# Optimization experiments

Measured on AMD Instinct MI355X. Metric: run time of the kernel, lower is better.

Reference implementation:

```python
import jax, jax.numpy as jnp
import numpy as np

B, T, D = 8, 2048, 1024  # batch, seq (== block_size), n_embd == head_size


def setup_inputs() -> dict:
    key = jax.random.key(0)
    k0, k1, k2, k3 = jax.random.split(key, 4)
    s = 1.0 / np.sqrt(D)
    return {
        "x": jax.random.normal(k0, (B, T, D), dtype=jnp.float32),
        "Wk": jax.random.normal(k1, (D, D), dtype=jnp.float32) * s,
        "Wq": jax.random.normal(k2, (D, D), dtype=jnp.float32) * s,
        "Wv": jax.random.normal(k3, (D, D), dtype=jnp.float32) * s,
    }


def reference(x, Wk, Wq, Wv):
    Bb, Tt, C = x.shape
    k = jnp.einsum("btc,ch->bth", x, Wk)
    q = jnp.einsum("btc,ch->bth", x, Wq)
    v = jnp.einsum("btc,ch->bth", x, Wv)
    # scaled dot-product scores with causal (tril) mask; scale = C**-0.5 (n_embd)
    wei = jnp.einsum("bqh,bkh->bqk", q, k) * (1.0 / jnp.sqrt(jnp.float32(C)))
    causal = jnp.tril(jnp.ones((Tt, Tt), dtype=bool))
    wei = jnp.where(causal[None, :, :], wei, jnp.float32(-jnp.inf))
    wei = jax.nn.softmax(wei, axis=-1)
    # dropout is identity in eval mode
    out = jnp.einsum("bqk,bkh->bqh", wei, v)
    return out
```

## Files before the change

kernel.cpp:

```cpp
#include <hip/hip_runtime.h>
#include <hip/hip_bf16.h>

#define BB 8
#define TT 2048
#define DD 1024

typedef __attribute__((ext_vector_type(8))) short short8;
typedef __attribute__((ext_vector_type(4))) float f32x4;
typedef __attribute__((ext_vector_type(4))) unsigned short u16x4;

__device__ inline void gload_lds16(const void* g, void* l) {
    __builtin_amdgcn_global_load_lds((const __attribute__((address_space(1))) void*)g,
                                     (__attribute__((address_space(3))) void*)l, 16, 0, 0);
}

#define VMW4 asm volatile("s_waitcnt vmcnt(4)" ::: "memory")
#define VMW0 asm volatile("s_waitcnt vmcnt(0)" ::: "memory")
#define BARX() __builtin_amdgcn_s_barrier()

#define MM_PAIR(NF0)                                                          \
    do {                                                                      \
        __builtin_amdgcn_s_setprio(1);                                        \
        _Pragma("unroll")                                                     \
        for (int mf = 0; mf < 8; mf++) {                                      \
            acc[mf][NF0] = __builtin_amdgcn_mfma_f32_16x16x32_bf16(           \
                aF[mf], bF[NF0], acc[mf][NF0], 0, 0, 0);                      \
            acc[mf][NF0 + 1] = __builtin_amdgcn_mfma_f32_16x16x32_bf16(       \
                aF[mf], bF[NF0 + 1], acc[mf][NF0 + 1], 0, 0, 0);              \
        }                                                                     \
        __builtin_amdgcn_s_setprio(0);                                        \
    } while (0)

template<int MODE, typename CT>
__device__ __forceinline__ void gemm_core256(
    const __hip_bfloat16* __restrict__ A,
    const __hip_bfloat16* __restrict__ Bt,
    void* __restrict__ Cbase,
    int lda, int ldb, int ldc,
    int m0, int n0, int kmax,
    float scale, float* __restrict__ rs)
{
    __shared__ __align__(16) char lsA[65536];
    __shared__ __align__(16) char lsB[65536];

    const int t   = threadIdx.x;
    const int w   = t >> 6;
    const int l   = t & 63;
    const int q   = l >> 4;
    const int i16 = l & 15;
    const int wy  = w >> 2;
    const int wx  = w & 3;

    const int r0  = w * 32 + (l >> 2);
    const int r1  = r0 + 16;
    const int cg0 = (l & 3) ^ ((r0 >> 1) & 3);
    const int cg1 = (l & 3) ^ ((r1 >> 1) & 3);
    const __hip_bfloat16* gA0 = A  + (size_t)(m0 + r0) * lda + cg0 * 8;
    const __hip_bfloat16* gA1 = A  + (size_t)(m0 + r1) * lda + cg1 * 8;
    const __hip_bfloat16* gB0 = Bt + (size_t)(n0 + r0) * ldb + cg0 * 8;
    const __hip_bfloat16* gB1 = Bt + (size_t)(n0 + r1) * ldb + cg1 * 8;

    const int swz  = (q ^ ((i16 >> 1) & 3)) << 4;
    const int offA = (wy * 128 + i16) * 64 + swz;
    const int offB = (wx * 64  + i16) * 64 + swz;

    f32x4 acc[8][4];
#pragma unroll
    for (int mf = 0; mf < 8; mf++)
#pragma unroll
        for (int nf = 0; nf < 4; nf++) acc[mf][nf] = f32x4{0.f, 0.f, 0.f, 0.f};

    short8 aF[8], bF[4];
    const int NT = kmax >> 6;

    {
        char* dA = lsA + (w << 11);
        char* dB = lsB + (w << 11);
        gload_lds16(gA0, dA);            gload_lds16(gA1, dA + 1024);
        gload_lds16(gB0, dB);            gload_lds16(gB1, dB + 1024);
        gload_lds16(gA0 + 32, dA + 16384); gload_lds16(gA1 + 32, dA + 16384 + 1024);
        gload_lds16(gB0 + 32, dB + 16384); gload_lds16(gB1 + 32, dB + 16384 + 1024);
    }
    VMW4; BARX();

    int buf = 0;
    for (int tt = 0; tt < NT; ++tt, buf ^= 1) {
        const bool nx = (tt + 1) < NT;
        const int  kn = (tt + 1) << 6;
        char* sA = lsA + (buf ? 32768 : 0);
        char* sB = lsB + (buf ? 32768 : 0);
        char* dA = lsA + (buf ? 0 : 32768) + (w << 11);
        char* dB = lsB + (buf ? 0 : 32768) + (w << 11);

#pragma unroll
        for (int mf = 0; mf < 8; mf++)
            aF[mf] = *(const short8*)(sA + offA + mf * 1024);
#pragma unroll
        for (int nf = 0; nf < 4; nf++)
            bF[nf] = *(const short8*)(sB + offB + nf * 1024);
        if (nx) { gload_lds16(gA0 + kn, dA); gload_lds16(gA1 + kn, dA + 1024); }
        BARX();
        MM_PAIR(0);
        BARX();
        if (nx) { gload_lds16(gB0 + kn, dB); gload_lds16(gB1 + kn, dB + 1024); }
        BARX();
        MM_PAIR(2);
        if (nx) { VMW4; } else { VMW0; }
        BARX();
#pragma unroll
        for (int mf = 0; mf < 8; mf++)
            aF[mf] = *(const short8*)(sA + 16384 + offA + mf * 1024);
#pragma unroll
        for (int nf = 0; nf < 4; nf++)
            bF[nf] = *(const short8*)(sB + 16384 + offB + nf * 1024);
        if (nx) { gload_lds16(gA0 + kn + 32, dA + 16384);
                  gload_lds16(gA1 + kn + 32, dA + 16384 + 1024); }
        BARX();
        MM_PAIR(0);
        BARX();
        if (nx) { gload_lds16(gB0 + kn + 32, dB + 16384);
                  gload_lds16(gB1 + kn + 32, dB + 16384 + 1024); }
        BARX();
        MM_PAIR(2);
        if (nx) { VMW4; }
        BARX();
    }

    if constexpr (MODE == 0) {
        CT* C = (CT*)Cbase;
#pragma unroll
        for (int mf = 0; mf < 8; mf++) {
            int rbase = m0 + wy * 128 + mf * 16 + q * 4;
#pragma unroll
            for (int nf = 0; nf < 4; nf++) {
                int col = n0 + wx * 64 + nf * 16 + i16;
#pragma unroll
                for (int r = 0; r < 4; r++) {
                    float v = acc[mf][nf][r] * scale;
                    if constexpr (sizeof(CT) == 2)
                        C[(size_t)(rbase + r) * ldc + col] = (CT)__float2bfloat16(v);
                    else
                        *((float*)&C[(size_t)(rbase + r) * ldc + col]) = v;
                }
            }
        }
    } else if constexpr (MODE == 1) {
        __hip_bfloat16* C = (__hip_bfloat16*)Cbase;
#pragma unroll
        for (int mf = 0; mf < 8; mf++) {
            int rbase = m0 + wy * 128 + mf * 16 + q * 4;
#pragma unroll
            for (int r = 0; r < 4; r++) {
                int row = rbase + r;
                float part = 0.f, pv[4];
#pragma unroll
                for (int nf = 0; nf < 4; nf++) {
                    int col = n0 + wx * 64 + nf * 16 + i16;
                    float e = (col <= row) ? __expf(acc[mf][nf][r] * scale) : 0.f;
                    pv[nf] = e;
                    part += e;
                }
                part += __shfl_xor(part, 1, 64);
                part += __shfl_xor(part, 2, 64);
                part += __shfl_xor(part, 4, 64);
                part += __shfl_xor(part, 8, 64);
                if (i16 == 0) atomicAdd(&rs[row], part);
#pragma unroll
                for (int nf = 0; nf < 4; nf++) {
                    int col = n0 + wx * 64 + nf * 16 + i16;
                    C[(size_t)row * ldc + col] = __float2bfloat16(pv[nf]);
                }
            }
        }
    } else {
        float* C = (float*)Cbase;
#pragma unroll
        for (int mf = 0; mf < 8; mf++) {
            int rbase = m0 + wy * 128 + mf * 16 + q * 4;
#pragma unroll
            for (int r = 0; r < 4; r++) {
                int row = rbase + r;
                float inv = 1.f / rs[row];
#pragma unroll
                for (int nf = 0; nf < 4; nf++) {
                    int col = n0 + wx * 64 + nf * 16 + i16;
                    C[(size_t)row * ldc + col] = acc[mf][nf][r] * inv;
                }
            }
        }
    }
}

__global__ __launch_bounds__(512, 2) void proj3_8ph(
    const __hip_bfloat16* __restrict__ xb,
    const __hip_bfloat16* __restrict__ wt,
    __hip_bfloat16* __restrict__ kq,
    __hip_bfloat16* __restrict__ vT2)
{
    const int z = blockIdx.y;
    const int x = blockIdx.x;
    const int swz = (x & 7) * 32 + (x >> 3);
    const __hip_bfloat16 *A, *Bt;
    void* C;
    int ldc, m0, n0;
    if (z < 2) {
        A = xb; Bt = wt + z * 1048576; C = kq + (size_t)z * 16777216;
        ldc = 1024; m0 = (swz >> 2) * 256; n0 = (swz & 3) * 256;
    } else {
        A = wt + 2 * 1048576; Bt = xb; C = vT2;
        ldc = 16384; m0 = (swz & 3) * 256; n0 = (swz >> 2) * 256;
    }
    gemm_core256<0, __hip_bfloat16>(A, Bt, C, 1024, 1024, ldc, m0, n0, 1024, 1.0f, nullptr);
}

__global__ __launch_bounds__(512, 2) void sgemm256(
    const __hip_bfloat16* __restrict__ qq,
    const __hip_bfloat16* __restrict__ kk,
    __hip_bfloat16* __restrict__ Pp,
    float* __restrict__ rsum)
{
    const int z = blockIdx.z;
    const int y = blockIdx.y;
    const int ne = ((y + z) & 1) ? blockIdx.x : 7 - blockIdx.x;
    if (ne > y) return;
    gemm_core256<1, __hip_bfloat16>(
        qq + (size_t)z * 2097152, kk + (size_t)z * 2097152,
        Pp + (size_t)z * 4194304,
        1024, 1024, 2048, y * 256, ne * 256, 1024, 0.03125f,
        rsum + (size_t)z * TT);
}

__global__ __launch_bounds__(512, 2) void pvgemm256(
    const __hip_bfloat16* __restrict__ Pp,
    const __hip_bfloat16* __restrict__ vT2,
    float* __restrict__ out,
    float* __restrict__ rsum)
{
    const int z = blockIdx.z;
    const int y = blockIdx.y;
    const int x = blockIdx.x;
    gemm_core256<2, float>(
        Pp + (size_t)z * 4194304, vT2 + (size_t)z * 2048,
        out + (size_t)z * 2097152,
        2048, 16384, 1024, y * 256, x * 256, (y + 1) * 256, 1.0f,
        rsum + (size_t)z * TT);
}

__global__ __launch_bounds__(256) void cvt_x(const float* __restrict__ in,
                                             unsigned short* __restrict__ out)
{
    size_t i = ((size_t)blockIdx.x * 256 + threadIdx.x) * 4;
    float4 f = *(const float4*)(in + i);
    union { u16x4 u; __hip_bfloat16 h[4]; } o;
    o.h[0] = __float2bfloat16(f.x);
    o.h[1] = __float2bfloat16(f.y);
    o.h[2] = __float2bfloat16(f.z);
    o.h[3] = __float2bfloat16(f.w);
    *(u16x4*)(out + i) = o.u;
}

__global__ __launch_bounds__(256) void transpose_cvt_w(
    const float* __restrict__ Wk, const float* __restrict__ Wq,
    const float* __restrict__ Wv, __hip_bfloat16* __restrict__ Wt)
{
    const float* W = blockIdx.z == 0 ? Wk : (blockIdx.z == 1 ? Wq : Wv);
    __hip_bfloat16* o = Wt + (size_t)blockIdx.z * DD * DD;
    int h0 = blockIdx.x * 32, c0 = blockIdx.y * 32;
    __shared__ float tl[32][33];
    int tx = threadIdx.x, ty = threadIdx.y;
#pragma unroll
    for (int k = 0; k < 4; k++)
        tl[ty + 8 * k][tx] = W[(size_t)(c0 + ty + 8 * k) * DD + h0 + tx];
    __syncthreads();
#pragma unroll
    for (int k = 0; k < 4; k++)
        o[(size_t)(h0 + ty + 8 * k) * DD + c0 + tx] = __float2bfloat16(tl[tx][ty + 8 * k]);
}

extern "C" void kernel_launch(void* const* d_in, const int* in_sizes, int n_in,
                              void* d_out, int out_size, void* d_ws, size_t ws_size,
                              hipStream_t stream)
{
    const float* x  = (const float*)d_in[0];
    const float* Wk = (const float*)d_in[1];
    const float* Wq = (const float*)d_in[2];
    const float* Wv = (const float*)d_in[3];
    float* out = (float*)d_out;

    char* ws = (char*)d_ws;
    __hip_bfloat16* kk   = (__hip_bfloat16*)ws;
    __hip_bfloat16* qq   = (__hip_bfloat16*)(ws + 33554432);
    __hip_bfloat16* vT2  = (__hip_bfloat16*)(ws + 67108864);
    __hip_bfloat16* wt   = (__hip_bfloat16*)(ws + 100663296);
    float*          rsum = (float*)         (ws + 100663296);
    __hip_bfloat16* xb   = (__hip_bfloat16*)(ws + 106954752);
    __hip_bfloat16* Pp   = (__hip_bfloat16*)(ws + 106954752);

    int g = (ws_size >= 106954752ull + 8ull * 8388608ull) ? 8 : 4;

    cvt_x<<<16384, 256, 0, stream>>>(x, (unsigned short*)xb);
    transpose_cvt_w<<<dim3(32, 32, 3), dim3(32, 8), 0, stream>>>(Wk, Wq, Wv, wt);

    proj3_8ph<<<dim3(256, 3), 512, 0, stream>>>(xb, wt, kk, vT2);

    for (int g0 = 0; g0 < BB; g0 += g) {
        hipMemsetAsync(rsum, 0, (size_t)g * TT * 4, stream);

        sgemm256<<<dim3(8, 8, g), 512, 0, stream>>>(
            qq + (size_t)g0 * 2097152, kk + (size_t)g0 * 2097152, Pp, rsum);

        pvgemm256<<<dim3(4, 8, g), 512, 0, stream>>>(
            Pp, vT2 + (size_t)g0 * 2048, out + (size_t)g0 * 2097152, rsum);
    }
}
```

Baseline: 369.4 us.

## Restructure GEMM main loop into register double-buffered ping-pong pipeline

Rewrites the shared bf16 GEMM core loop so A fragments are double-buffered in registers (aF0/aF1), with global-to-LDS prefetch of half-tiles interleaved between full 8x4 MFMA blocks. The barrier count per k-step drops from eight to two, and sched_barrier fences keep the loads and MFMAs in separate phases. Leading dimensions become template constants so address arithmetic folds at compile time. In exchange, register pressure rises and the schedule clamps prefetch indices at the tail, which means redundant loads on the last iterations. The loop also assumes NT is even.

New measurement: 407.2 us. 1.1x slower.

```diff
diff --git a/kernel.cpp b/kernel.cpp
--- a/kernel.cpp
+++ b/kernel.cpp
@@ -14,30 +14,16 @@
                                      (__attribute__((address_space(3))) void*)l, 16, 0, 0);
 }
 
-#define VMW4 asm volatile("s_waitcnt vmcnt(4)" ::: "memory")
-#define VMW0 asm volatile("s_waitcnt vmcnt(0)" ::: "memory")
+#define VMW(N) asm volatile("s_waitcnt vmcnt(" #N ")" ::: "memory")
 #define BARX() __builtin_amdgcn_s_barrier()
-
-#define MM_PAIR(NF0)                                                          \
-    do {                                                                      \
-        __builtin_amdgcn_s_setprio(1);                                        \
-        _Pragma("unroll")                                                     \
-        for (int mf = 0; mf < 8; mf++) {                                      \
-            acc[mf][NF0] = __builtin_amdgcn_mfma_f32_16x16x32_bf16(           \
-                aF[mf], bF[NF0], acc[mf][NF0], 0, 0, 0);                      \
-            acc[mf][NF0 + 1] = __builtin_amdgcn_mfma_f32_16x16x32_bf16(       \
-                aF[mf], bF[NF0 + 1], acc[mf][NF0 + 1], 0, 0, 0);              \
-        }                                                                     \
-        __builtin_amdgcn_s_setprio(0);                                        \
-    } while (0)
-
-template<int MODE, typename CT>
+#define SCHEDB() __builtin_amdgcn_sched_barrier(0)
+
+template<int MODE, typename CT, int LDA, int LDB>
 __device__ __forceinline__ void gemm_core256(
     const __hip_bfloat16* __restrict__ A,
     const __hip_bfloat16* __restrict__ Bt,
     void* __restrict__ Cbase,
-    int lda, int ldb, int ldc,
-    int m0, int n0, int kmax,
+    int ldc, int m0, int n0, int kmax,
     float scale, float* __restrict__ rs)
 {
     __shared__ __align__(16) char lsA[65536];
@@ -55,10 +41,11 @@
     const int r1  = r0 + 16;
     const int cg0 = (l & 3) ^ ((r0 >> 1) & 3);
     const int cg1 = (l & 3) ^ ((r1 >> 1) & 3);
-    const __hip_bfloat16* gA0 = A  + (size_t)(m0 + r0) * lda + cg0 * 8;
-    const __hip_bfloat16* gA1 = A  + (size_t)(m0 + r1) * lda + cg1 * 8;
-    const __hip_bfloat16* gB0 = Bt + (size_t)(n0 + r0) * ldb + cg0 * 8;
-    const __hip_bfloat16* gB1 = Bt + (size_t)(n0 + r1) * ldb + cg1 * 8;
+    const __hip_bfloat16* gA0 = A  + (size_t)(m0 + r0) * LDA + cg0 * 8;
+    const __hip_bfloat16* gA1 = A  + (size_t)(m0 + r1) * LDA + cg1 * 8;
+    const __hip_bfloat16* gB0 = Bt + (size_t)(n0 + r0) * LDB + cg0 * 8;
+    const __hip_bfloat16* gB1 = Bt + (size_t)(n0 + r1) * LDB + cg1 * 8;
+    const int dw = w << 11;
 
     const int swz  = (q ^ ((i16 >> 1) & 3)) << 4;
     const int offA = (wy * 128 + i16) * 64 + swz;
@@ -70,61 +57,85 @@
 #pragma unroll
         for (int nf = 0; nf < 4; nf++) acc[mf][nf] = f32x4{0.f, 0.f, 0.f, 0.f};
 
-    short8 aF[8], bF[4];
+    short8 aF0[8], aF1[8], bF[4];
     const int NT = kmax >> 6;
 
     {
-        char* dA = lsA + (w << 11);
-        char* dB = lsB + (w << 11);
-        gload_lds16(gA0, dA);            gload_lds16(gA1, dA + 1024);
-        gload_lds16(gB0, dB);            gload_lds16(gB1, dB + 1024);
-        gload_lds16(gA0 + 32, dA + 16384); gload_lds16(gA1 + 32, dA + 16384 + 1024);
-        gload_lds16(gB0 + 32, dB + 16384); gload_lds16(gB1 + 32, dB + 16384 + 1024);
-    }
-    VMW4; BARX();
-
-    int buf = 0;
-    for (int tt = 0; tt < NT; ++tt, buf ^= 1) {
-        const bool nx = (tt + 1) < NT;
-        const int  kn = (tt + 1) << 6;
-        char* sA = lsA + (buf ? 32768 : 0);
-        char* sB = lsB + (buf ? 32768 : 0);
-        char* dA = lsA + (buf ? 0 : 32768) + (w << 11);
-        char* dB = lsB + (buf ? 0 : 32768) + (w << 11);
-
-#pragma unroll
-        for (int mf = 0; mf < 8; mf++)
-            aF[mf] = *(const short8*)(sA + offA + mf * 1024);
-#pragma unroll
-        for (int nf = 0; nf < 4; nf++)
-            bF[nf] = *(const short8*)(sB + offB + nf * 1024);
-        if (nx) { gload_lds16(gA0 + kn, dA); gload_lds16(gA1 + kn, dA + 1024); }
-        BARX();
-        MM_PAIR(0);
-        BARX();
-        if (nx) { gload_lds16(gB0 + kn, dB); gload_lds16(gB1 + kn, dB + 1024); }
-        BARX();
-        MM_PAIR(2);
-        if (nx) { VMW4; } else { VMW0; }
-        BARX();
-#pragma unroll
-        for (int mf = 0; mf < 8; mf++)
-            aF[mf] = *(const short8*)(sA + 16384 + offA + mf * 1024);
-#pragma unroll
-        for (int nf = 0; nf < 4; nf++)
-            bF[nf] = *(const short8*)(sB + 16384 + offB + nf * 1024);
-        if (nx) { gload_lds16(gA0 + kn + 32, dA + 16384);
-                  gload_lds16(gA1 + kn + 32, dA + 16384 + 1024); }
-        BARX();
-        MM_PAIR(0);
-        BARX();
-        if (nx) { gload_lds16(gB0 + kn + 32, dB + 16384);
-                  gload_lds16(gB1 + kn + 32, dB + 16384 + 1024); }
-        BARX();
-        MM_PAIR(2);
-        if (nx) { VMW4; }
-        BARX();
-    }
+        gload_lds16(gA0, lsA + dw);           gload_lds16(gA1, lsA + dw + 1024);
+        gload_lds16(gA0 + 32, lsA + 16384 + dw);
+        gload_lds16(gA1 + 32, lsA + 16384 + dw + 1024);
+        gload_lds16(gB0, lsB + dw);           gload_lds16(gB1, lsB + dw + 1024);
+        gload_lds16(gB0 + 32, lsB + 16384 + dw);
+        gload_lds16(gB1 + 32, lsB + 16384 + dw + 1024);
+        const int kp = (1 < NT ? 1 : NT - 1) << 6;
+        gload_lds16(gA0 + kp, lsA + 32768 + dw);
+        gload_lds16(gA1 + kp, lsA + 32768 + dw + 1024);
+    }
+    VMW(8); BARX();
+#pragma unroll
+    for (int mf = 0; mf < 8; mf++)
+        aF0[mf] = *(const short8*)(lsA + offA + mf * 1024);
+    VMW(4); BARX();
+
+    for (int tt = 0; tt < NT; tt += 2) {
+#pragma unroll
+        for (int bb = 0; bb < 2; bb++) {
+            const int ti = tt + bb;
+            char* sA = lsA + (bb ? 32768 : 0);
+            char* sB = lsB + (bb ? 32768 : 0);
+            char* oA = lsA + (bb ? 0 : 32768);
+            char* oB = lsB + (bb ? 0 : 32768);
+            const int tn1 = (ti + 1 < NT) ? ti + 1 : NT - 1;
+            const int tn2 = (ti + 2 < NT) ? ti + 2 : NT - 1;
+            const int kn1 = tn1 << 6;
+            const int kn2 = tn2 << 6;
+
+#pragma unroll
+            for (int nf = 0; nf < 4; nf++)
+                bF[nf] = *(const short8*)(sB + offB + nf * 1024);
+#pragma unroll
+            for (int mf = 0; mf < 8; mf++)
+                aF1[mf] = *(const short8*)(sA + 16384 + offA + mf * 1024);
+            gload_lds16(gA0 + kn1 + 32, oA + 16384 + dw);
+            gload_lds16(gA1 + kn1 + 32, oA + 16384 + dw + 1024);
+            gload_lds16(gB0 + kn1, oB + dw);
+            gload_lds16(gB1 + kn1, oB + dw + 1024);
+            SCHEDB();
+            __builtin_amdgcn_s_setprio(1);
+#pragma unroll
+            for (int mf = 0; mf < 8; mf++)
+#pragma unroll
+                for (int nf = 0; nf < 4; nf++)
+                    acc[mf][nf] = __builtin_amdgcn_mfma_f32_16x16x32_bf16(
+                        aF0[mf], bF[nf], acc[mf][nf], 0, 0, 0);
+            __builtin_amdgcn_s_setprio(0);
+            SCHEDB();
+            VMW(4); BARX();
+
+#pragma unroll
+            for (int nf = 0; nf < 4; nf++)
+                bF[nf] = *(const short8*)(sB + 16384 + offB + nf * 1024);
+#pragma unroll
+            for (int mf = 0; mf < 8; mf++)
+                aF0[mf] = *(const short8*)(oA + offA + mf * 1024);
+            gload_lds16(gB0 + kn1 + 32, oB + 16384 + dw);
+            gload_lds16(gB1 + kn1 + 32, oB + 16384 + dw + 1024);
+            gload_lds16(gA0 + kn2, sA + dw);
+            gload_lds16(gA1 + kn2, sA + dw + 1024);
+            SCHEDB();
+            __builtin_amdgcn_s_setprio(1);
+#pragma unroll
+            for (int mf = 0; mf < 8; mf++)
+#pragma unroll
+                for (int nf = 0; nf < 4; nf++)
+                    acc[mf][nf] = __builtin_amdgcn_mfma_f32_16x16x32_bf16(
+                        aF1[mf], bF[nf], acc[mf][nf], 0, 0, 0);
+            __builtin_amdgcn_s_setprio(0);
+            SCHEDB();
+            VMW(4); BARX();
+        }
+    }
+    VMW(0);
 
     if constexpr (MODE == 0) {
         CT* C = (CT*)Cbase;
@@ -210,7 +221,8 @@
         A = wt + 2 * 1048576; Bt = xb; C = vT2;
         ldc = 16384; m0 = (swz & 3) * 256; n0 = (swz >> 2) * 256;
     }
-    gemm_core256<0, __hip_bfloat16>(A, Bt, C, 1024, 1024, ldc, m0, n0, 1024, 1.0f, nullptr);
+    gemm_core256<0, __hip_bfloat16, 1024, 1024>(A, Bt, C, ldc, m0, n0, 1024,
+                                                1.0f, nullptr);
 }
 
 __global__ __launch_bounds__(512, 2) void sgemm256(
@@ -223,10 +235,10 @@
     const int y = blockIdx.y;
     const int ne = ((y + z) & 1) ? blockIdx.x : 7 - blockIdx.x;
     if (ne > y) return;
-    gemm_core256<1, __hip_bfloat16>(
+    gemm_core256<1, __hip_bfloat16, 1024, 1024>(
         qq + (size_t)z * 2097152, kk + (size_t)z * 2097152,
         Pp + (size_t)z * 4194304,
-        1024, 1024, 2048, y * 256, ne * 256, 1024, 0.03125f,
+        2048, y * 256, ne * 256, 1024, 0.03125f,
         rsum + (size_t)z * TT);
 }
 
@@ -239,10 +251,10 @@
     const int z = blockIdx.z;
     const int y = blockIdx.y;
     const int x = blockIdx.x;
-    gemm_core256<2, float>(
+    gemm_core256<2, float, 2048, 16384>(
         Pp + (size_t)z * 4194304, vT2 + (size_t)z * 2048,
         out + (size_t)z * 2097152,
-        2048, 16384, 1024, y * 256, x * 256, (y + 1) * 256, 1.0f,
+        1024, y * 256, x * 256, (y + 1) * 256, 1.0f,
         rsum + (size_t)z * TT);
 }
 
```
